# Kernel tuning notes

Hardware: AMD Instinct MI355X
Metric: run time of the kernel (lower is better)

## Reference

```python
import jax, jax.numpy as jnp
import numpy as np

N, E, T, D, C = 20000, 160000, 3, 128, 128  # nodes, edges, replicas, in=out feat dim, num_classes
NUM_EDGES = 128  # linear1 output width (must be <= C for the H scatter to be in-range)


def setup_inputs() -> dict:
    key = jax.random.key(0)
    ks = jax.random.split(key, 8)
    s = 1.0 / np.sqrt(D)
    return {
        "edge_index": jax.random.randint(ks[0], (2, E), 0, N, dtype=jnp.int32),
        "features": jax.random.normal(ks[1], (N, D), jnp.float32),
        "lin_W": jax.random.normal(ks[2], (T, D, D), jnp.float32) * s,   # t per-replica Linears
        "lin_b": jnp.zeros((T, D), jnp.float32),
        "gcn1_W": jax.random.normal(ks[3], (D, C), jnp.float32) * s,
        "gcn1_b": jnp.zeros((C,), jnp.float32),
        "gcn2_W": jax.random.normal(ks[4], (C, C), jnp.float32) * s,
        "gcn2_b": jnp.zeros((C,), jnp.float32),
        "lin1_W": jax.random.normal(ks[5], (C, NUM_EDGES), jnp.float32) * s,
        "lin1_b": jnp.zeros((NUM_EDGES,), jnp.float32),
    }


def _gcn(x, W, b, src, dst, n):
    """PyG GCNConv: add self-loops, symmetric deg^-1/2 normalization, scatter-add."""
    loop = jnp.arange(n, dtype=src.dtype)
    src = jnp.concatenate([src, loop])
    dst = jnp.concatenate([dst, loop])
    deg = jax.ops.segment_sum(jnp.ones(src.shape, x.dtype), dst, num_segments=n)
    dinv = jax.lax.rsqrt(deg)  # deg >= 1 because of self-loops
    norm = dinv[src] * dinv[dst]
    xw = x @ W
    return jax.ops.segment_sum(xw[src] * norm[:, None], dst, num_segments=n) + b


def reference(edge_index, features, lin_W, lin_b, gcn1_W, gcn1_b, gcn2_W, gcn2_b, lin1_W, lin1_b):
    src, dst = edge_index[0], edge_index[1]
    n = features.shape[0]
    t = lin_W.shape[0]
    scale = features.shape[1] ** -0.5  # out_features ** -0.5
    # t linear replicas, concatenated along nodes -> [t*n, D]
    transformed = (jnp.einsum('nd,tde->tne', features, lin_W) + lin_b[:, None, :]).reshape(t * n, -1)
    # replicate-selection via cosine similarity (exact torch index order:
    # src.repeat_interleave(t) vs dst.repeat(t))
    rep_src = jnp.repeat(src, t)
    exp_dst = jnp.tile(dst, t)
    a = features[rep_src]
    bb = transformed[exp_dst]
    sim = (a * bb).sum(-1) / jnp.maximum(
        jnp.linalg.norm(a, axis=-1) * jnp.linalg.norm(bb, axis=-1), 1e-8)
    best = jnp.argmax(sim.reshape(-1, t), axis=1)            # [E]
    best_nodes = dst + best.astype(dst.dtype) * n            # index into replica blocks
    # extra edges: (arange(n), arange(n) + i*n) for i in range(t)
    extra_src = jnp.tile(jnp.arange(n, dtype=src.dtype), t)
    extra_dst = (jnp.arange(n, dtype=src.dtype)[None, :]
                 + (jnp.arange(t, dtype=src.dtype) * n)[:, None]).reshape(-1)
    src_all = jnp.concatenate([src, src, extra_src])
    dst_all = jnp.concatenate([dst, best_nodes, extra_dst])
    nt = (t + 1) * n
    all_features = jnp.concatenate([features, transformed], axis=0)  # [(t+1)n, D]
    # GCN backbone (dropout = identity in eval mode)
    h = jax.nn.relu(all_features)
    h = jax.nn.relu(_gcn(h, gcn1_W, gcn1_b, src_all, dst_all, nt))
    all_features2 = _gcn(h, gcn2_W, gcn2_b, src_all, dst_all, nt)    # [(t+1)n, C]
    logits = jax.nn.relu(all_features2) @ lin1_W + lin1_b            # [(t+1)n, NUM_EDGES]
    num_classes = gcn2_b.shape[0]
    classes = jnp.argmax(logits.reshape(t + 1, n, -1), axis=-1)      # [t+1, n]
    H = jax.nn.one_hot(classes, num_classes, dtype=features.dtype).sum(0)  # [n, C] vote counts
    # per-class segment sum over nodes with H[:, j] > 0 (only first n rows are ever selected)
    mask = (H > 0).astype(features.dtype)                            # [n, C]
    hyperedge_features = mask.T @ all_features2[:n]                  # [C, D]
    dots = (all_features @ hyperedge_features.T) * scale             # [(t+1)n, C]
    H = jax.nn.softmax(H, axis=0)
    return H, hyperedge_features, dots
```

## Files before the change

kernel.cpp:

```cpp
#include <hip/hip_runtime.h>
#include <math.h>

#define NN 20000
#define NE 160000
#define TT 3
#define DD 128
#define NTOT 80000
#define N3 60000
#define NBLK1 79

__device__ __forceinline__ float waveReduceSum(float v) {
#pragma unroll
  for (int off = 32; off >= 1; off >>= 1)
    v += __shfl_xor(v, off, 64);
  return v;
}

__device__ __forceinline__ void atomAddF(float* p, float v) {
  unsafeAtomicAdd(p, v);
}

__global__ __launch_bounds__(256) void k_copy_feat(const float* __restrict__ src,
                                                   float* __restrict__ dst, int n4) {
  int i = blockIdx.x * 256 + threadIdx.x;
  if (i < n4) ((float4*)dst)[i] = ((const float4*)src)[i];
}

template <int RELU_IN, int TRANS_W, int DO_ARGMAX>
__global__ __launch_bounds__(256, 2) void gemm128(const float* __restrict__ X,
                                                  const float* __restrict__ W,
                                                  const float* __restrict__ bias,
                                                  float* __restrict__ out, int M,
                                                  float scale, int wStride, int bStride,
                                                  long oStride, int* __restrict__ cls) {
  __shared__ float Ws[128 * 132];
  const int tid = threadIdx.x;
  const int rbase = blockIdx.x * 128;
  W += (long)blockIdx.y * wStride;
  if (bias) bias += (long)blockIdx.y * bStride;
  out += (long)blockIdx.y * oStride;

#pragma unroll
  for (int it = 0; it < 16; ++it) {
    int idx = (tid + it * 256) * 4;
    int kl = idx >> 7, c = idx & 127;
    float4 w;
    if (!TRANS_W) {
      w = *(const float4*)&W[kl * 128 + c];
    } else {
      w.x = W[(c + 0) * 128 + kl];
      w.y = W[(c + 1) * 128 + kl];
      w.z = W[(c + 2) * 128 + kl];
      w.w = W[(c + 3) * 128 + kl];
    }
    *(float4*)&Ws[kl * 132 + c] = w;
  }

  const int tc = tid & 15, tr = tid >> 4;
  const int c0 = tc * 8, r0 = tr * 8;

  const float4* xrow[8];
#pragma unroll
  for (int i = 0; i < 8; ++i) {
    int gr = rbase + r0 + i;
    int gc = (gr < M) ? gr : 0;
    xrow[i] = (const float4*)(X + (long)gc * 128);
  }

  float acc[8][8];
#pragma unroll
  for (int i = 0; i < 8; ++i)
#pragma unroll
    for (int j = 0; j < 8; ++j) acc[i][j] = 0.f;

  float4 xc[8], xn[8];
#pragma unroll
  for (int i = 0; i < 8; ++i) {
    float4 v = xrow[i][0];
    if (RELU_IN) {
      v.x = fmaxf(v.x, 0.f);
      v.y = fmaxf(v.y, 0.f);
      v.z = fmaxf(v.z, 0.f);
      v.w = fmaxf(v.w, 0.f);
    }
    xc[i] = v;
  }

  __syncthreads();

  for (int kq = 0; kq < 32; ++kq) {
    if (kq < 31) {
#pragma unroll
      for (int i = 0; i < 8; ++i) {
        float4 v = xrow[i][kq + 1];
        if (RELU_IN) {
          v.x = fmaxf(v.x, 0.f);
          v.y = fmaxf(v.y, 0.f);
          v.z = fmaxf(v.z, 0.f);
          v.w = fmaxf(v.w, 0.f);
        }
        xn[i] = v;
      }
    }
    const int klb = kq * 4;
#pragma unroll
    for (int k = 0; k < 4; ++k) {
      const int kl = klb + k;
      const float4 wa = *(const float4*)&Ws[kl * 132 + c0];
      const float4 wb = *(const float4*)&Ws[kl * 132 + c0 + 4];
      float av[8];
#pragma unroll
      for (int i = 0; i < 8; ++i)
        av[i] = (k == 0) ? xc[i].x : (k == 1) ? xc[i].y : (k == 2) ? xc[i].z : xc[i].w;
      const float bv[8] = {wa.x, wa.y, wa.z, wa.w, wb.x, wb.y, wb.z, wb.w};
#pragma unroll
      for (int i = 0; i < 8; ++i)
#pragma unroll
        for (int j = 0; j < 8; ++j) acc[i][j] = fmaf(av[i], bv[j], acc[i][j]);
    }
    if (kq < 31) {
#pragma unroll
      for (int i = 0; i < 8; ++i) xc[i] = xn[i];
    }
  }

  float bb[8];
#pragma unroll
  for (int j = 0; j < 8; ++j) bb[j] = 0.f;
  if (bias) {
#pragma unroll
    for (int j = 0; j < 8; ++j) bb[j] = bias[c0 + j];
  }

  if (DO_ARGMAX) {
#pragma unroll
    for (int i = 0; i < 8; ++i) {
      float bv = acc[i][0] * scale + bb[0];
      int bc = c0;
#pragma unroll
      for (int j = 1; j < 8; ++j) {
        float v = acc[i][j] * scale + bb[j];
        if (v > bv) {
          bv = v;
          bc = c0 + j;
        }
      }
#pragma unroll
      for (int off = 1; off <= 8; off <<= 1) {
        float ov = __shfl_xor(bv, off, 64);
        int oc = __shfl_xor(bc, off, 64);
        if (ov > bv || (ov == bv && oc < bc)) {
          bv = ov;
          bc = oc;
        }
      }
      int gr = rbase + r0 + i;
      if (tc == 0 && gr < M) cls[gr] = bc;
    }
  } else {
#pragma unroll
    for (int i = 0; i < 8; ++i) {
      int gr = rbase + r0 + i;
      if (gr < M) {
        float4 v0, v1;
        v0.x = acc[i][0] * scale + bb[0];
        v0.y = acc[i][1] * scale + bb[1];
        v0.z = acc[i][2] * scale + bb[2];
        v0.w = acc[i][3] * scale + bb[3];
        v1.x = acc[i][4] * scale + bb[4];
        v1.y = acc[i][5] * scale + bb[5];
        v1.z = acc[i][6] * scale + bb[6];
        v1.w = acc[i][7] * scale + bb[7];
        *(float4*)&out[(long)gr * 128 + c0] = v0;
        *(float4*)&out[(long)gr * 128 + c0 + 4] = v1;
      }
    }
  }
}

__global__ __launch_bounds__(256) void k_norms(const float* __restrict__ feat,
                                               const float* __restrict__ A,
                                               float* __restrict__ nf,
                                               float* __restrict__ nt0) {
  int w = blockIdx.x * 4 + (threadIdx.x >> 6);
  int lane = threadIdx.x & 63;
  if (w >= 2 * NN) return;
  const float* p = (w < NN) ? (feat + (long)w * 128) : (A + (long)(NN + (w - NN)) * 128);
  float v0 = p[lane], v1 = p[lane + 64];
  float s = waveReduceSum(v0 * v0 + v1 * v1);
  if (lane == 0) {
    float r = sqrtf(s);
    if (w < NN) nf[w] = r;
    else nt0[w - NN] = r;
  }
}

__global__ __launch_bounds__(256) void k_sim(const int* __restrict__ ei,
                                             const float* __restrict__ feat,
                                             const float* __restrict__ A,
                                             const float* __restrict__ nf,
                                             const float* __restrict__ nt0,
                                             int* __restrict__ bn) {
  int e = blockIdx.x * 4 + (threadIdx.x >> 6);
  int lane = threadIdx.x & 63;
  if (e >= NE) return;
  int s = ei[e];
  const float* fp = feat + (long)s * 128;
  float a0 = fp[lane], a1 = fp[lane + 64];
  float na = nf[s];
  float bv = 0.f;
  int bk = 0;
#pragma unroll
  for (int k = 0; k < 3; ++k) {
    int j = 3 * e + k;
    if (j >= NE) j -= NE;
    if (j >= NE) j -= NE;
    int d = ei[NE + j];
    const float* bp = A + (long)(NN + d) * 128;
    float dot = waveReduceSum(a0 * bp[lane] + a1 * bp[lane + 64]);
    float sim = dot / fmaxf(na * nt0[d], 1e-8f);
    if (k == 0 || sim > bv) {
      bv = sim;
      bk = k;
    }
  }
  if (lane == 0) bn[e] = ei[NE + e] + bk * NN;
}

__global__ __launch_bounds__(256) void k_zero_count(int* __restrict__ count) {
  int v = blockIdx.x * 256 + threadIdx.x;
  if (v < NTOT) count[v] = 0;
}

__global__ __launch_bounds__(256) void k_count(const int* __restrict__ ei,
                                               const int* __restrict__ bn,
                                               int* __restrict__ count) {
  int e = blockIdx.x * 256 + threadIdx.x;
  if (e < NE) {
    atomicAdd(&count[ei[NE + e]], 1);
    atomicAdd(&count[bn[e]], 1);
  }
}

__global__ __launch_bounds__(256) void k_dinv(const int* __restrict__ count,
                                              float* __restrict__ dinv) {
  int v = blockIdx.x * 256 + threadIdx.x;
  if (v < NTOT) {
    float deg = (float)count[v] + ((v < N3) ? 2.f : 1.f);
    dinv[v] = 1.f / sqrtf(deg);
  }
}

__global__ __launch_bounds__(256) void k_scan1(const int* __restrict__ count,
                                               int* __restrict__ start,
                                               int* __restrict__ bsum) {
  __shared__ int sh[256];
  const int b = blockIdx.x, t = threadIdx.x;
  const int base = b * 1024 + t * 4;
  int c[4];
  int s = 0;
#pragma unroll
  for (int k = 0; k < 4; ++k) {
    int idx = base + k;
    c[k] = (idx < NTOT) ? count[idx] : 0;
    s += c[k];
  }
  sh[t] = s;
  __syncthreads();
  for (int off = 1; off < 256; off <<= 1) {
    int v = (t >= off) ? sh[t - off] : 0;
    __syncthreads();
    sh[t] += v;
    __syncthreads();
  }
  if (t == 255) bsum[b] = sh[255];
  int run = sh[t] - s;
#pragma unroll
  for (int k = 0; k < 4; ++k) {
    int idx = base + k;
    if (idx < NTOT) start[idx] = run;
    run += c[k];
  }
}

__global__ __launch_bounds__(256) void k_scan2(int* __restrict__ bsum) {
  __shared__ int sh[256];
  const int t = threadIdx.x;
  int v = (t < NBLK1) ? bsum[t] : 0;
  sh[t] = v;
  __syncthreads();
  for (int off = 1; off < 256; off <<= 1) {
    int u = (t >= off) ? sh[t - off] : 0;
    __syncthreads();
    sh[t] += u;
    __syncthreads();
  }
  if (t < NBLK1) bsum[t] = sh[t] - v;
}

__global__ __launch_bounds__(256) void k_scan3(int* __restrict__ start,
                                               const int* __restrict__ bsum,
                                               int* __restrict__ cursor) {
  int i = blockIdx.x * 256 + threadIdx.x;
  if (i < NTOT) {
    int v = start[i] + bsum[i >> 10];
    start[i] = v;
    cursor[i] = v;
  }
}

__global__ __launch_bounds__(256) void k_fill(const int* __restrict__ ei,
                                              const int* __restrict__ bn,
                                              const float* __restrict__ dinv,
                                              int* __restrict__ cursor,
                                              int2* __restrict__ ent) {
  int g = blockIdx.x * 256 + threadIdx.x;
  if (g >= 2 * NE) return;
  int e = (g < NE) ? g : g - NE;
  int s = ei[e];
  int d = (g < NE) ? ei[NE + e] : bn[e];
  float w = dinv[s] * dinv[d];
  int pos = atomicAdd(&cursor[d], 1);
  ent[pos] = make_int2(s, __float_as_int(w));
}

__global__ __launch_bounds__(256) void k_agg(const int2* __restrict__ ent,
                                             const int* __restrict__ start,
                                             const int* __restrict__ end,
                                             const float* __restrict__ xw,
                                             const float* __restrict__ dinv,
                                             const float* __restrict__ bias,
                                             float* __restrict__ out) {
  int v = blockIdx.x * 4 + (threadIdx.x >> 6);
  int lane = threadIdx.x & 63;
  float dv = dinv[v];
  const float* xr = xw + (long)v * 128;
  float b0 = xr[lane], b1 = xr[lane + 64];
  float acc0 = bias[lane] + dv * dv * b0;
  float acc1 = bias[lane + 64] + dv * dv * b1;
  if (v < NN) {
    acc0 += dv * dv * b0;
    acc1 += dv * dv * b1;
  } else if (v < N3) {
    int j = (v < 2 * NN) ? v - NN : v - 2 * NN;
    const float* xj = xw + (long)j * 128;
    float w = dinv[j] * dv;
    acc0 = fmaf(w, xj[lane], acc0);
    acc1 = fmaf(w, xj[lane + 64], acc1);
  }
  const int i1 = end[v];
  int i = start[v];
  if (i < i1) {
    int2 en = ent[i];
    for (; i < i1; ++i) {
      int2 nx = en;
      if (i + 1 < i1) nx = ent[i + 1];
      float w = __int_as_float(en.y);
      const float* xs = xw + (long)en.x * 128;
      acc0 = fmaf(w, xs[lane], acc0);
      acc1 = fmaf(w, xs[lane + 64], acc1);
      en = nx;
    }
  }
  out[(long)v * 128 + lane] = acc0;
  out[(long)v * 128 + lane + 64] = acc1;
}

__global__ __launch_bounds__(256) void k_zero_small(float* __restrict__ hyper,
                                                    int* __restrict__ hist) {
  int i = blockIdx.x * 256 + threadIdx.x;
  if (i < 128 * 128) hyper[i] = 0.f;
  if (i < 640) hist[i] = 0;
}

#define HISTBLK 20
__global__ __launch_bounds__(256) void k_hist(const int* __restrict__ cls,
                                              int* __restrict__ hist) {
  __shared__ int sh[640];
  const int t = threadIdx.x;
  for (int i = t; i < 640; i += 256) sh[i] = 0;
  __syncthreads();
  const int per = NN / HISTBLK;
  const int j0 = blockIdx.x * per;
  for (int j = j0 + t; j < j0 + per; j += 256) {
    int cc[4] = {cls[j], cls[NN + j], cls[2 * NN + j], cls[3 * NN + j]};
#pragma unroll
    for (int i = 0; i < 4; ++i) {
      bool first = true;
      int m = 0;
#pragma unroll
      for (int k = 0; k < 4; ++k) {
        if (cc[k] == cc[i]) {
          if (k < i) first = false;
          m++;
        }
      }
      if (first) atomicAdd(&sh[cc[i] * 5 + m], 1);
    }
  }
  __syncthreads();
  for (int i = t; i < 640; i += 256) {
    int v = sh[i];
    if (v) atomicAdd(&hist[i], v);
  }
}

__global__ void k_table(const int* __restrict__ hist, float* __restrict__ table) {
  int c = threadIdx.x;
  if (c >= 128) return;
  int cnt[5];
  int tot = 0;
  for (int v = 1; v <= 4; ++v) {
    cnt[v] = hist[c * 5 + v];
    tot += cnt[v];
  }
  cnt[0] = NN - tot;
  int m = 0;
  for (int v = 0; v <= 4; ++v)
    if (cnt[v] > 0) m = v;
  float ex[5];
  float denom = 0.f;
  for (int v = 0; v <= 4; ++v) {
    ex[v] = expf((float)(v - m));
    denom += (float)cnt[v] * ex[v];
  }
  for (int v = 0; v <= 4; ++v) table[c * 5 + v] = ex[v] / denom;
}

__global__ __launch_bounds__(256) void k_hwrite(const int* __restrict__ cls,
                                                const float* __restrict__ table,
                                                float* __restrict__ H) {
  int j = blockIdx.x * 2 + (threadIdx.x >> 7);
  int c = threadIdx.x & 127;
  if (j >= NN) return;
  int c0 = cls[j], c1 = cls[NN + j], c2 = cls[2 * NN + j], c3 = cls[3 * NN + j];
  int cnt = (c == c0) + (c == c1) + (c == c2) + (c == c3);
  H[(long)j * 128 + c] = table[c * 5 + cnt];
}

#define HBLK 250
#define HPER 80
__global__ __launch_bounds__(256) void k_hyper(const int* __restrict__ cls,
                                               const float* __restrict__ af2,
                                               float* __restrict__ hyper) {
  __shared__ float acc[128 * 128];
  const int t = threadIdx.x;
  for (int i = t; i < 128 * 128; i += 256) acc[i] = 0.f;
  __syncthreads();
  const int j0 = blockIdx.x * HPER;
  const int j1 = j0 + HPER;
  const int d = t & 127;
  const int half = t >> 7;
  float v = af2[(long)j0 * 128 + d];
  int c0 = cls[j0], c1 = cls[NN + j0], c2 = cls[2 * NN + j0], c3 = cls[3 * NN + j0];
  for (int j = j0; j < j1; ++j) {
    float vn = 0.f;
    int n0 = 0, n1 = 0, n2 = 0, n3 = 0;
    if (j + 1 < j1) {
      vn = af2[(long)(j + 1) * 128 + d];
      n0 = cls[j + 1];
      n1 = cls[NN + j + 1];
      n2 = cls[2 * NN + j + 1];
      n3 = cls[3 * NN + j + 1];
    }
    if (half == 0) {
      atomicAdd(&acc[c0 * 128 + d], v);
      if (c2 != c0 && c2 != c1) atomicAdd(&acc[c2 * 128 + d], v);
    } else {
      if (c1 != c0) atomicAdd(&acc[c1 * 128 + d], v);
      if (c3 != c0 && c3 != c1 && c3 != c2) atomicAdd(&acc[c3 * 128 + d], v);
    }
    v = vn;
    c0 = n0;
    c1 = n1;
    c2 = n2;
    c3 = n3;
  }
  __syncthreads();
  for (int i = t; i < 128 * 128; i += 256) {
    float x = acc[i];
    if (x != 0.f) atomAddF(&hyper[i], x);
  }
}

extern "C" void kernel_launch(void* const* d_in, const int* in_sizes, int n_in,
                              void* d_out, int out_size, void* d_ws, size_t ws_size,
                              hipStream_t stream) {
  (void)in_sizes;
  (void)n_in;
  (void)out_size;
  (void)ws_size;
  const int* ei = (const int*)d_in[0];
  const float* feat = (const float*)d_in[1];
  const float* lin_W = (const float*)d_in[2];
  const float* lin_b = (const float*)d_in[3];
  const float* g1W = (const float*)d_in[4];
  const float* g1b = (const float*)d_in[5];
  const float* g2W = (const float*)d_in[6];
  const float* g2b = (const float*)d_in[7];
  const float* l1W = (const float*)d_in[8];
  const float* l1b = (const float*)d_in[9];

  float* out = (float*)d_out;
  float* H = out;
  float* hyper = out + (size_t)NN * 128;
  float* dots = hyper + 128 * 128;

  float* ws = (float*)d_ws;
  float* A = ws;
  float* Cb = A + (size_t)NTOT * 128;
  float* Bb = dots;
  float* dinv = Cb + (size_t)NTOT * 128;
  float* nf = dinv + NTOT;
  float* nt0 = nf + NN;
  int* bn = (int*)(nt0 + NN);
  int* cls = bn + NE;
  int* hist = cls + NTOT;
  float* table = (float*)(hist + 640);
  int* count = (int*)(table + 640);
  int* startA = count + NTOT;
  int* cursor = startA + NTOT;
  int* bsum = cursor + NTOT;
  int2* ent = (int2*)(bsum + 128);

  const float kScale = 0.08838834764831843f;

  k_copy_feat<<<(NN * 128 / 4 + 255) / 256, 256, 0, stream>>>(feat, A, NN * 128 / 4);
  gemm128<0, 0, 0><<<dim3(157, 3), 256, 0, stream>>>(
      feat, lin_W, lin_b, A + (size_t)NN * 128, NN, 1.f, 128 * 128, 128,
      (long)NN * 128, nullptr);
  k_norms<<<10000, 256, 0, stream>>>(feat, A, nf, nt0);
  k_zero_count<<<(NTOT + 255) / 256, 256, 0, stream>>>(count);
  k_sim<<<NE / 4, 256, 0, stream>>>(ei, feat, A, nf, nt0, bn);
  k_count<<<(NE + 255) / 256, 256, 0, stream>>>(ei, bn, count);
  k_dinv<<<(NTOT + 255) / 256, 256, 0, stream>>>(count, dinv);
  k_scan1<<<NBLK1, 256, 0, stream>>>(count, startA, bsum);
  k_scan2<<<1, 256, 0, stream>>>(bsum);
  k_scan3<<<(NTOT + 255) / 256, 256, 0, stream>>>(startA, bsum, cursor);
  k_fill<<<(2 * NE + 255) / 256, 256, 0, stream>>>(ei, bn, dinv, cursor, ent);
  gemm128<1, 0, 0><<<dim3(NTOT / 128, 1), 256, 0, stream>>>(A, g1W, nullptr, Bb, NTOT,
                                                            1.f, 0, 0, 0, nullptr);
  k_agg<<<NTOT / 4, 256, 0, stream>>>(ent, startA, cursor, Bb, dinv, g1b, Cb);
  gemm128<1, 0, 0><<<dim3(NTOT / 128, 1), 256, 0, stream>>>(Cb, g2W, nullptr, Bb, NTOT,
                                                            1.f, 0, 0, 0, nullptr);
  k_agg<<<NTOT / 4, 256, 0, stream>>>(ent, startA, cursor, Bb, dinv, g2b, Cb);
  gemm128<1, 0, 1><<<dim3(NTOT / 128, 1), 256, 0, stream>>>(Cb, l1W, l1b, nullptr,
                                                            NTOT, 1.f, 0, 0, 0, cls);
  k_zero_small<<<64, 256, 0, stream>>>(hyper, hist);
  k_hist<<<HISTBLK, 256, 0, stream>>>(cls, hist);
  k_table<<<1, 128, 0, stream>>>(hist, table);
  k_hwrite<<<NN / 2, 256, 0, stream>>>(cls, table, H);
  k_hyper<<<HBLK, 256, 0, stream>>>(cls, Cb, hyper);
  gemm128<0, 1, 0><<<dim3(NTOT / 128, 1), 256, 0, stream>>>(A, hyper, nullptr, dots,
                                                            NTOT, kScale, 0, 0, 0,
                                                            nullptr);
}
```

Measured before the change: 474.2 us.

## Split 128-col GEMM tiles into two 64-col halves for higher occupancy

The shared 128x128 GEMM now computes a 128x64 output tile per block, using a third grid dimension to select the column half. This halves the shared memory and accumulator registers per block, and launch bounds now ask for four resident blocks instead of two, so more waves can hide latency. The fused argmax now writes a per-half (value, class) pair, and a new small merge kernel picks the final class. In exchange, every X row tile is loaded twice from global memory, and there is one extra launch plus a small intermediate buffer.

```diff
diff --git a/kernel.cpp b/kernel.cpp
--- a/kernel.cpp
+++ b/kernel.cpp
@@ -27,56 +27,52 @@
 }
 
 template <int RELU_IN, int TRANS_W, int DO_ARGMAX>
-__global__ __launch_bounds__(256, 2) void gemm128(const float* __restrict__ X,
+__global__ __launch_bounds__(256, 4) void gemm128(const float* __restrict__ X,
                                                   const float* __restrict__ W,
                                                   const float* __restrict__ bias,
                                                   float* __restrict__ out, int M,
                                                   float scale, int wStride, int bStride,
-                                                  long oStride, int* __restrict__ cls) {
-  __shared__ float Ws[128 * 132];
+                                                  long oStride,
+                                                  float2* __restrict__ abuf) {
+  __shared__ float Ws[128 * 68];
   const int tid = threadIdx.x;
   const int rbase = blockIdx.x * 128;
+  const int z = blockIdx.z;
   W += (long)blockIdx.y * wStride;
   if (bias) bias += (long)blockIdx.y * bStride;
   out += (long)blockIdx.y * oStride;
 
 #pragma unroll
-  for (int it = 0; it < 16; ++it) {
-    int idx = (tid + it * 256) * 4;
-    int kl = idx >> 7, c = idx & 127;
-    float4 w;
+  for (int it = 0; it < 8; ++it) {
+    int e = tid + it * 256;
     if (!TRANS_W) {
-      w = *(const float4*)&W[kl * 128 + c];
+      int kl = e >> 4, c = (e & 15) * 4;
+      *(float4*)&Ws[kl * 68 + c] = *(const float4*)&W[kl * 128 + z * 64 + c];
     } else {
-      w.x = W[(c + 0) * 128 + kl];
-      w.y = W[(c + 1) * 128 + kl];
-      w.z = W[(c + 2) * 128 + kl];
-      w.w = W[(c + 3) * 128 + kl];
-    }
-    *(float4*)&Ws[kl * 132 + c] = w;
+      int c = e & 63, klb = (e >> 6) * 4;
+      float4 w = *(const float4*)&W[(long)(z * 64 + c) * 128 + klb];
+      Ws[(klb + 0) * 68 + c] = w.x;
+      Ws[(klb + 1) * 68 + c] = w.y;
+      Ws[(klb + 2) * 68 + c] = w.z;
+      Ws[(klb + 3) * 68 + c] = w.w;
+    }
   }
 
   const int tc = tid & 15, tr = tid >> 4;
-  const int c0 = tc * 8, r0 = tr * 8;
-
-  const float4* xrow[8];
+  const int c0 = tc * 4, r0 = tr * 8;
+  const int grb = rbase + r0;
+  const float* __restrict__ xb = X + (long)((grb < M) ? grb : 0) * 128;
+
+  float acc[8][4];
+#pragma unroll
+  for (int i = 0; i < 8; ++i)
+#pragma unroll
+    for (int j = 0; j < 4; ++j) acc[i][j] = 0.f;
+
+  float4 xc[8], xn[8];
 #pragma unroll
   for (int i = 0; i < 8; ++i) {
-    int gr = rbase + r0 + i;
-    int gc = (gr < M) ? gr : 0;
-    xrow[i] = (const float4*)(X + (long)gc * 128);
-  }
-
-  float acc[8][8];
-#pragma unroll
-  for (int i = 0; i < 8; ++i)
-#pragma unroll
-    for (int j = 0; j < 8; ++j) acc[i][j] = 0.f;
-
-  float4 xc[8], xn[8];
-#pragma unroll
-  for (int i = 0; i < 8; ++i) {
-    float4 v = xrow[i][0];
+    float4 v = *(const float4*)&xb[i * 128];
     if (RELU_IN) {
       v.x = fmaxf(v.x, 0.f);
       v.y = fmaxf(v.y, 0.f);
@@ -92,7 +88,7 @@
     if (kq < 31) {
 #pragma unroll
       for (int i = 0; i < 8; ++i) {
-        float4 v = xrow[i][kq + 1];
+        float4 v = *(const float4*)&xb[i * 128 + (kq + 1) * 4];
         if (RELU_IN) {
           v.x = fmaxf(v.x, 0.f);
           v.y = fmaxf(v.y, 0.f);
@@ -102,21 +98,18 @@
         xn[i] = v;
       }
     }
-    const int klb = kq * 4;
 #pragma unroll
     for (int k = 0; k < 4; ++k) {
-      const int kl = klb + k;
-      const float4 wa = *(const float4*)&Ws[kl * 132 + c0];
-      const float4 wb = *(const float4*)&Ws[kl * 132 + c0 + 4];
-      float av[8];
-#pragma unroll
-      for (int i = 0; i < 8; ++i)
-        av[i] = (k == 0) ? xc[i].x : (k == 1) ? xc[i].y : (k == 2) ? xc[i].z : xc[i].w;
-      const float bv[8] = {wa.x, wa.y, wa.z, wa.w, wb.x, wb.y, wb.z, wb.w};
-#pragma unroll
-      for (int i = 0; i < 8; ++i)
-#pragma unroll
-        for (int j = 0; j < 8; ++j) acc[i][j] = fmaf(av[i], bv[j], acc[i][j]);
+      const float4 w4 = *(const float4*)&Ws[(kq * 4 + k) * 68 + c0];
+#pragma unroll
+      for (int i = 0; i < 8; ++i) {
+        float a = (k == 0) ? xc[i].x : (k == 1) ? xc[i].y : (k == 2) ? xc[i].z
+                                                                     : xc[i].w;
+        acc[i][0] = fmaf(a, w4.x, acc[i][0]);
+        acc[i][1] = fmaf(a, w4.y, acc[i][1]);
+        acc[i][2] = fmaf(a, w4.z, acc[i][2]);
+        acc[i][3] = fmaf(a, w4.w, acc[i][3]);
+      }
     }
     if (kq < 31) {
 #pragma unroll
@@ -124,25 +117,25 @@
     }
   }
 
-  float bb[8];
-#pragma unroll
-  for (int j = 0; j < 8; ++j) bb[j] = 0.f;
+  float bb[4];
+#pragma unroll
+  for (int j = 0; j < 4; ++j) bb[j] = 0.f;
   if (bias) {
 #pragma unroll
-    for (int j = 0; j < 8; ++j) bb[j] = bias[c0 + j];
+    for (int j = 0; j < 4; ++j) bb[j] = bias[z * 64 + c0 + j];
   }
 
   if (DO_ARGMAX) {
 #pragma unroll
     for (int i = 0; i < 8; ++i) {
       float bv = acc[i][0] * scale + bb[0];
-      int bc = c0;
-#pragma unroll
-      for (int j = 1; j < 8; ++j) {
+      int bc = z * 64 + c0;
+#pragma unroll
+      for (int j = 1; j < 4; ++j) {
         float v = acc[i][j] * scale + bb[j];
         if (v > bv) {
           bv = v;
-          bc = c0 + j;
+          bc = z * 64 + c0 + j;
         }
       }
 #pragma unroll
@@ -155,26 +148,30 @@
         }
       }
       int gr = rbase + r0 + i;
-      if (tc == 0 && gr < M) cls[gr] = bc;
+      if (tc == 0 && gr < M) abuf[(long)z * M + gr] = make_float2(bv, (float)bc);
     }
   } else {
 #pragma unroll
     for (int i = 0; i < 8; ++i) {
       int gr = rbase + r0 + i;
       if (gr < M) {
-        float4 v0, v1;
-        v0.x = acc[i][0] * scale + bb[0];
-        v0.y = acc[i][1] * scale + bb[1];
-        v0.z = acc[i][2] * scale + bb[2];
-        v0.w = acc[i][3] * scale + bb[3];
-        v1.x = acc[i][4] * scale + bb[4];
-        v1.y = acc[i][5] * scale + bb[5];
-        v1.z = acc[i][6] * scale + bb[6];
-        v1.w = acc[i][7] * scale + bb[7];
-        *(float4*)&out[(long)gr * 128 + c0] = v0;
-        *(float4*)&out[(long)gr * 128 + c0 + 4] = v1;
+        float4 v;
+        v.x = acc[i][0] * scale + bb[0];
+        v.y = acc[i][1] * scale + bb[1];
+        v.z = acc[i][2] * scale + bb[2];
+        v.w = acc[i][3] * scale + bb[3];
+        *(float4*)&out[(long)gr * 128 + z * 64 + c0] = v;
       }
     }
+  }
+}
+
+__global__ __launch_bounds__(256) void k_amerge(const float2* __restrict__ abuf,
+                                                int* __restrict__ cls, int n) {
+  int i = blockIdx.x * 256 + threadIdx.x;
+  if (i < n) {
+    float2 a = abuf[i], b = abuf[(long)n + i];
+    cls[i] = (b.x > a.x) ? (int)b.y : (int)a.y;
   }
 }
 
@@ -522,11 +519,12 @@
   int* cursor = startA + NTOT;
   int* bsum = cursor + NTOT;
   int2* ent = (int2*)(bsum + 128);
+  float2* abuf = (float2*)(ent + 2 * NE);
 
   const float kScale = 0.08838834764831843f;
 
   k_copy_feat<<<(NN * 128 / 4 + 255) / 256, 256, 0, stream>>>(feat, A, NN * 128 / 4);
-  gemm128<0, 0, 0><<<dim3(157, 3), 256, 0, stream>>>(
+  gemm128<0, 0, 0><<<dim3(157, 3, 2), 256, 0, stream>>>(
       feat, lin_W, lin_b, A + (size_t)NN * 128, NN, 1.f, 128 * 128, 128,
       (long)NN * 128, nullptr);
   k_norms<<<10000, 256, 0, stream>>>(feat, A, nf, nt0);
@@ -538,20 +536,20 @@
   k_scan2<<<1, 256, 0, stream>>>(bsum);
   k_scan3<<<(NTOT + 255) / 256, 256, 0, stream>>>(startA, bsum, cursor);
   k_fill<<<(2 * NE + 255) / 256, 256, 0, stream>>>(ei, bn, dinv, cursor, ent);
-  gemm128<1, 0, 0><<<dim3(NTOT / 128, 1), 256, 0, stream>>>(A, g1W, nullptr, Bb, NTOT,
-                                                            1.f, 0, 0, 0, nullptr);
+  gemm128<1, 0, 0><<<dim3(NTOT / 128, 1, 2), 256, 0, stream>>>(
+      A, g1W, nullptr, Bb, NTOT, 1.f, 0, 0, 0, nullptr);
   k_agg<<<NTOT / 4, 256, 0, stream>>>(ent, startA, cursor, Bb, dinv, g1b, Cb);
-  gemm128<1, 0, 0><<<dim3(NTOT / 128, 1), 256, 0, stream>>>(Cb, g2W, nullptr, Bb, NTOT,
-                                                            1.f, 0, 0, 0, nullptr);
+  gemm128<1, 0, 0><<<dim3(NTOT / 128, 1, 2), 256, 0, stream>>>(
+      Cb, g2W, nullptr, Bb, NTOT, 1.f, 0, 0, 0, nullptr);
   k_agg<<<NTOT / 4, 256, 0, stream>>>(ent, startA, cursor, Bb, dinv, g2b, Cb);
-  gemm128<1, 0, 1><<<dim3(NTOT / 128, 1), 256, 0, stream>>>(Cb, l1W, l1b, nullptr,
-                                                            NTOT, 1.f, 0, 0, 0, cls);
+  gemm128<1, 0, 1><<<dim3(NTOT / 128, 1, 2), 256, 0, stream>>>(
+      Cb, l1W, l1b, nullptr, NTOT, 1.f, 0, 0, 0, abuf);
+  k_amerge<<<(NTOT + 255) / 256, 256, 0, stream>>>(abuf, cls, NTOT);
   k_zero_small<<<64, 256, 0, stream>>>(hyper, hist);
   k_hist<<<HISTBLK, 256, 0, stream>>>(cls, hist);
   k_table<<<1, 128, 0, stream>>>(hist, table);
   k_hwrite<<<NN / 2, 256, 0, stream>>>(cls, table, H);
   k_hyper<<<HBLK, 256, 0, stream>>>(cls, Cb, hyper);
-  gemm128<0, 1, 0><<<dim3(NTOT / 128, 1), 256, 0, stream>>>(A, hyper, nullptr, dots,
-                                                            NTOT, kScale, 0, 0, 0,
-                                                            nullptr);
-}
+  gemm128<0, 1, 0><<<dim3(NTOT / 128, 1, 2), 256, 0, stream>>>(
+      A, hyper, nullptr, dots, NTOT, kScale, 0, 0, 0, nullptr);
+}
```

Result: slower. 650.0 us (+37.1%).
